# Performance work log

Hardware: AMD Instinct MI355X
Metric: run time of the kernel (lower is better)

The kernel has to match this reference:

```python
import jax, jax.numpy as jnp
import numpy as np

B, T, C, H, S = 8, 2048, 1024, 16, 64
EPS = 1e-5


def layernorm(x, g, b):
    m = jnp.mean(x, axis=-1, keepdims=True)
    v = jnp.mean((x - m) ** 2, axis=-1, keepdims=True)
    return (x - m) * jax.lax.rsqrt(v + EPS) * g + b


def wkv6(r, k, v, time_decay, u):
    # r,k,v: [B,T,H,S]; time_decay,u: [H,S]
    # kernel receives ew=-exp(w) and uses decay = exp(ew) = exp(-exp(w))
    d = jnp.exp(-jnp.exp(time_decay))  # [H,S], in (0,1)

    def step(state, rkv):
        r_t, k_t, v_t = rkv  # each [B,H,S]
        kv = k_t[..., :, None] * v_t[..., None, :]  # [B,H,S,S] outer product
        y = jnp.einsum('bhk,bhkv->bhv', r_t, state + u[None, :, :, None] * kv)
        state = state * d[None, :, :, None] + kv
        return state, y

    s0 = jnp.zeros((B, H, S, S), r.dtype)
    rkv_tm = (jnp.moveaxis(r, 1, 0), jnp.moveaxis(k, 1, 0), jnp.moveaxis(v, 1, 0))
    _, ys = jax.lax.scan(step, s0, rkv_tm)  # ys: [T,B,H,S]
    return jnp.moveaxis(ys, 0, 1).reshape(B, T, C)


def setup_inputs() -> dict:
    key = jax.random.key(0)
    ks = jax.random.split(key, 10)
    sc = C ** -0.5
    return {
        'x': jax.random.normal(ks[0], (B, T, C), jnp.float32),
        'time_decay': -5.0 + 0.5 * jax.random.normal(ks[1], (H, S), jnp.float32),
        'time_first': 0.1 * jax.random.normal(ks[2], (H, S), jnp.float32),
        'w_r': sc * jax.random.normal(ks[3], (C, C), jnp.float32),
        'w_k': sc * jax.random.normal(ks[4], (C, C), jnp.float32),
        'w_v': sc * jax.random.normal(ks[5], (C, C), jnp.float32),
        'w_o': sc * jax.random.normal(ks[6], (C, C), jnp.float32),
        'w_fk': sc * jax.random.normal(ks[7], (C, 4 * C), jnp.float32),
        'w_fv': (4 * C) ** -0.5 * jax.random.normal(ks[8], (4 * C, C), jnp.float32),
        'g1': jnp.ones((C,), jnp.float32),
        'b1': jnp.zeros((C,), jnp.float32),
        'g2': jnp.ones((C,), jnp.float32),
        'b2': jnp.zeros((C,), jnp.float32),
    }


def reference(x, time_decay, time_first, w_r, w_k, w_v, w_o, w_fk, w_fv, g1, b1, g2, b2):
    x_ln = layernorm(x, g1, b1)
    r = (x_ln @ w_r).reshape(B, T, H, S)
    k = (x_ln @ w_k).reshape(B, T, H, S)
    v = (x_ln @ w_v).reshape(B, T, H, S)
    wkv = wkv6(r, k, v, time_decay, time_first)  # [B,T,C]
    rwkv = jax.nn.sigmoid(r.reshape(B, T, C)) * wkv
    x = x + rwkv @ w_o
    x_ln2 = layernorm(x, g2, b2)
    ffn = (jax.nn.relu(x_ln2 @ w_fk) ** 2) @ w_fv
    return x + ffn
```

## Files before the change

kernel.cpp:

```cpp
#include <hip/hip_runtime.h>
#include <hip/hip_bf16.h>

#define B_ 8
#define T_ 2048
#define C_ 1024
#define H_ 16
#define S_ 64
#define BT_ (B_*T_)
#define FF_ (4*C_)
#define NC_ 32

typedef __attribute__((ext_vector_type(8))) short short8;
typedef __attribute__((ext_vector_type(4))) float f32x4;

union U8 { uint4 v; unsigned short s[8]; };

static __device__ __forceinline__ unsigned short f2bf(float f){
  unsigned u = __float_as_uint(f);
  unsigned r = (u + 0x7fffu + ((u >> 16) & 1u)) >> 16;
  return (unsigned short)r;
}
static __device__ __forceinline__ float bf2f(unsigned short u){
  return __uint_as_float(((unsigned)u) << 16);
}

static __device__ __forceinline__ void gll16(const unsigned short* g, unsigned short* l){
  __builtin_amdgcn_global_load_lds((const __attribute__((address_space(1))) void*)g,
                                   (__attribute__((address_space(3))) void*)l, 16, 0, 0);
}

__global__ __launch_bounds__(256) void ln_kernel(const float* __restrict__ x,
    const float* __restrict__ g, const float* __restrict__ b,
    unsigned short* __restrict__ out){
  int row = blockIdx.x;
  int tid = threadIdx.x;
  const float4* xr = reinterpret_cast<const float4*>(x + (size_t)row * C_);
  float4 v = xr[tid];
  float s = v.x + v.y + v.z + v.w;
  float q = v.x*v.x + v.y*v.y + v.z*v.z + v.w*v.w;
  int lane = tid & 63, w = tid >> 6;
  #pragma unroll
  for (int off = 32; off; off >>= 1){ s += __shfl_down(s, off); q += __shfl_down(q, off); }
  __shared__ float red[2][4];
  if (lane == 0){ red[0][w] = s; red[1][w] = q; }
  __syncthreads();
  s = red[0][0] + red[0][1] + red[0][2] + red[0][3];
  q = red[1][0] + red[1][1] + red[1][2] + red[1][3];
  float mean = s * (1.0f / C_);
  float var  = q * (1.0f / C_) - mean * mean;
  float inv = rsqrtf(var + 1e-5f);
  float4 gg = reinterpret_cast<const float4*>(g)[tid];
  float4 bb = reinterpret_cast<const float4*>(b)[tid];
  ushort4 o;
  o.x = f2bf((v.x - mean) * inv * gg.x + bb.x);
  o.y = f2bf((v.y - mean) * inv * gg.y + bb.y);
  o.z = f2bf((v.z - mean) * inv * gg.z + bb.z);
  o.w = f2bf((v.w - mean) * inv * gg.w + bb.w);
  reinterpret_cast<ushort4*>(out + (size_t)row * C_)[tid] = o;
}

__global__ __launch_bounds__(256) void wconv_kernel(const float* __restrict__ w,
    unsigned short* __restrict__ wt, int K, int N){
  __shared__ float tile[32][33];
  int bk = blockIdx.x * 32, bn = blockIdx.y * 32;
  int tx = threadIdx.x & 31, ty = threadIdx.x >> 5;
  #pragma unroll
  for (int i = 0; i < 4; i++)
    tile[ty + 8*i][tx] = w[(size_t)(bk + ty + 8*i) * N + bn + tx];
  __syncthreads();
  #pragma unroll
  for (int i = 0; i < 4; i++)
    wt[(size_t)(bn + ty + 8*i) * K + bk + tx] = f2bf(tile[tx][ty + 8*i]);
}

#define EPI_RKV3 1
#define EPI_WO   2
#define EPI_FK   3
#define EPI_FV   4

template<int EPI>
__global__ __launch_bounds__(512, 2) void gemm64_kernel(
    const unsigned short* __restrict__ A,
    const unsigned short* __restrict__ Bt,
    void* __restrict__ outp,
    const float* __restrict__ aux,
    int K, int nx){
  __shared__ unsigned short As[2][256][64];
  __shared__ unsigned short Bs[2][256][64];
  const int tid = threadIdx.x;

  int nwg = gridDim.x;
  int id  = blockIdx.x;
  id = (id & 7) * (nwg >> 3) + (id >> 3);
  int gsz = nx << 2;
  int g = id / gsz, rem = id % gsz;
  const int bm = ((g << 2) + (rem & 3)) * 256;
  const int bn = (rem >> 2) * 256;

  const int lane = tid & 63, wid = tid >> 6;
  const int wr = wid >> 2, wc = wid & 3;
  const int ml = lane & 15, hi = lane >> 4;

  const int srow  = lane >> 3;
  const int gslot = (lane & 7) ^ srow;

  auto stageA13 = [&](int bf, int kt){
    const size_t ko = (size_t)kt * 64 + gslot * 8;
    gll16(A + (size_t)(bm +  64 + wid*8 + srow) * K + ko, &As[bf][ 64 + wid*8][0]);
    gll16(A + (size_t)(bm + 192 + wid*8 + srow) * K + ko, &As[bf][192 + wid*8][0]);
  };
  auto stageA02 = [&](int bf, int kt){
    const size_t ko = (size_t)kt * 64 + gslot * 8;
    gll16(A + (size_t)(bm +       wid*8 + srow) * K + ko, &As[bf][      wid*8][0]);
    gll16(A + (size_t)(bm + 128 + wid*8 + srow) * K + ko, &As[bf][128 + wid*8][0]);
  };
  auto stageB4 = [&](int bf, int kt){
    const size_t ko = (size_t)kt * 64 + gslot * 8;
    #pragma unroll
    for (int s = 0; s < 4; s++)
      gll16(Bt + (size_t)(bn + s*64 + wid*8 + srow) * K + ko, &Bs[bf][s*64 + wid*8][0]);
  };

  auto lda = [&](int bf, int mf, int kk) -> short8 {
    return *(const short8*)&As[bf][wr*128 + mf*16 + ml][(((kk<<2)+hi) ^ (ml&7)) << 3];
  };
  auto ldb = [&](int bf, int nf, int kk) -> short8 {
    return *(const short8*)&Bs[bf][wc*64 + nf*16 + ml][(((kk<<2)+hi) ^ (ml&7)) << 3];
  };

  f32x4 acc[8][4];
  #pragma unroll
  for (int i = 0; i < 8; i++)
    #pragma unroll
    for (int j = 0; j < 4; j++)
      acc[i][j] = (f32x4){0.f, 0.f, 0.f, 0.f};

  const int NT = K >> 6;
  stageA02(0, 0); stageB4(0, 0);
  stageA13(0, 0);
  stageA02(1, 1); stageB4(1, 1);
  asm volatile("s_waitcnt vmcnt(8)" ::: "memory");
  __builtin_amdgcn_s_barrier();

  for (int kt = 0; kt < NT; ++kt){
    const int bf = kt & 1, nbf = bf ^ 1;
    const int k1 = (kt+1 < NT) ? kt+1 : kt;
    const int k2 = (kt+2 < NT) ? kt+2 : kt;
    short8 bfr[2][4];
    #pragma unroll
    for (int kk = 0; kk < 2; kk++)
      #pragma unroll
      for (int nf = 0; nf < 4; nf++)
        bfr[kk][nf] = ldb(bf, nf, kk);
    short8 af0[2][4];
    #pragma unroll
    for (int kk = 0; kk < 2; kk++)
      #pragma unroll
      for (int mf = 0; mf < 4; mf++)
        af0[kk][mf] = lda(bf, mf, kk);
    stageA13(nbf, k1);
    __builtin_amdgcn_s_setprio(1);
    #pragma unroll
    for (int mf = 0; mf < 4; mf++)
      #pragma unroll
      for (int kk = 0; kk < 2; kk++)
        #pragma unroll
        for (int nf = 0; nf < 4; nf++)
          acc[mf][nf] = __builtin_amdgcn_mfma_f32_16x16x32_bf16(af0[kk][mf], bfr[kk][nf], acc[mf][nf], 0, 0, 0);
    __builtin_amdgcn_s_setprio(0);
    asm volatile("s_waitcnt vmcnt(8) lgkmcnt(0)" ::: "memory");
    __builtin_amdgcn_s_barrier();
    short8 af1[2][4];
    #pragma unroll
    for (int kk = 0; kk < 2; kk++)
      #pragma unroll
      for (int mf = 0; mf < 4; mf++)
        af1[kk][mf] = lda(bf, 4+mf, kk);
    stageA02(bf, k2);
    stageB4(bf, k2);
    __builtin_amdgcn_s_setprio(1);
    #pragma unroll
    for (int mf = 0; mf < 4; mf++)
      #pragma unroll
      for (int kk = 0; kk < 2; kk++)
        #pragma unroll
        for (int nf = 0; nf < 4; nf++)
          acc[4+mf][nf] = __builtin_amdgcn_mfma_f32_16x16x32_bf16(af1[kk][mf], bfr[kk][nf], acc[4+mf][nf], 0, 0, 0);
    __builtin_amdgcn_s_setprio(0);
    asm volatile("s_waitcnt vmcnt(8) lgkmcnt(0)" ::: "memory");
    __builtin_amdgcn_s_barrier();
  }
  asm volatile("s_waitcnt vmcnt(0)" ::: "memory");

  const int rbase = bm + wr*128 + hi*4;
  const int cbase = bn + wc*64 + ml;
  #pragma unroll
  for (int mf = 0; mf < 8; mf++){
    #pragma unroll
    for (int nf = 0; nf < 4; nf++){
      #pragma unroll
      for (int r = 0; r < 4; r++){
        int m = rbase + mf*16 + r;
        int n = cbase + nf*16;
        float vv = acc[mf][nf][r];
        if (EPI == EPI_RKV3){
          unsigned short* o = (unsigned short*)outp;
          int b = m >> 11, t = m & (T_ - 1);
          int which = n >> 10, h = (n >> 6) & (H_ - 1), s = n & (S_ - 1);
          o[(size_t)which * BT_ * C_ + (((size_t)(b * H_ + h)) * T_ + t) * S_ + s] = f2bf(vv);
        } else if (EPI == EPI_WO){
          float* o = (float*)outp;
          o[(size_t)m * C_ + n] = aux[(size_t)m * C_ + n] + vv;
        } else if (EPI == EPI_FK){
          unsigned short* o = (unsigned short*)outp;
          float rl = vv > 0.f ? vv : 0.f;
          o[(size_t)m * FF_ + n] = f2bf(rl * rl);
        } else {
          float* o = (float*)outp;
          o[(size_t)m * C_ + n] += vv;
        }
      }
    }
  }
}


__global__ __launch_bounds__(256) void wkv_p1(
    const unsigned short* __restrict__ kT, const unsigned short* __restrict__ vT,
    const float* __restrict__ td, unsigned short* __restrict__ AS){
  const int bid = blockIdx.x;
  const int bh = bid >> 5, c = bid & (NC_ - 1);
  const int h = bh & (H_ - 1);
  const int tid = threadIdx.x, lane = tid & 63, w = tid >> 6;
  __shared__ unsigned short kh[64][72];
  __shared__ unsigned short vt[64][72];
  __shared__ float eps[64];
  if (tid < 64) eps[tid] = expf(td[h * S_ + tid]);
  __syncthreads();
  const int t = tid >> 2, q = (tid & 3) * 16;
  const size_t base = ((size_t)bh * T_ + c * 64 + t) * S_ + q;
  U8 k0, k1, v0, v1;
  k0.v = *(const uint4*)(kT + base);  k1.v = *(const uint4*)(kT + base + 8);
  v0.v = *(const uint4*)(vT + base);  v1.v = *(const uint4*)(vT + base + 8);
  const float mt = -(float)(63 - t);
  #pragma unroll
  for (int j = 0; j < 8; j++){
    int k = q + j;
    kh[k][t] = f2bf(bf2f(k0.s[j]) * expf(mt * eps[k]));
    vt[k][t] = v0.s[j];
  }
  #pragma unroll
  for (int j = 0; j < 8; j++){
    int k = q + 8 + j;
    kh[k][t] = f2bf(bf2f(k1.s[j]) * expf(mt * eps[k]));
    vt[k][t] = v1.s[j];
  }
  __syncthreads();
  const int ml = lane & 15, klo = (lane >> 4) * 8;
  f32x4 acc[4];
  #pragma unroll
  for (int nf = 0; nf < 4; nf++) acc[nf] = (f32x4){0.f,0.f,0.f,0.f};
  #pragma unroll
  for (int ks = 0; ks < 2; ks++){
    short8 af = *(const short8*)&vt[w*16 + ml][ks*32 + klo];
    #pragma unroll
    for (int nf = 0; nf < 4; nf++){
      short8 bfr = *(const short8*)&kh[nf*16 + ml][ks*32 + klo];
      acc[nf] = __builtin_amdgcn_mfma_f32_16x16x32_bf16(af, bfr, acc[nf], 0, 0, 0);
    }
  }
  unsigned short* dst = AS + ((size_t)bid * 64 + w*16 + (lane >> 4) * 4) * 64;
  #pragma unroll
  for (int nf = 0; nf < 4; nf++)
    #pragma unroll
    for (int r = 0; r < 4; r++)
      dst[(size_t)r * 64 + nf*16 + ml] = f2bf(acc[nf][r]);
}

__global__ __launch_bounds__(256) void wkv_p2(
    unsigned short* __restrict__ AS, const float* __restrict__ td){
  const int bh = blockIdx.x >> 2, vs = blockIdx.x & 3;
  const int h = bh & (H_ - 1);
  const int tid = threadIdx.x;
  const int vo = tid >> 4, k4 = (tid & 15) * 4;
  const int v = vs * 16 + vo;
  float dL[4], S[4];
  #pragma unroll
  for (int j = 0; j < 4; j++){
    dL[j] = expf(-64.f * expf(td[h * S_ + k4 + j]));
    S[j] = 0.f;
  }
  const size_t rb = ((size_t)bh * NC_ * 64 + v) * 64 + k4;
  for (int c = 0; c < NC_; c++){
    unsigned short* p = AS + rb + (size_t)c * 4096;
    ushort4 A = *(const ushort4*)p;
    ushort4 o;
    o.x = f2bf(S[0]); o.y = f2bf(S[1]); o.z = f2bf(S[2]); o.w = f2bf(S[3]);
    *(ushort4*)p = o;
    S[0] = fmaf(S[0], dL[0], bf2f(A.x)); S[1] = fmaf(S[1], dL[1], bf2f(A.y));
    S[2] = fmaf(S[2], dL[2], bf2f(A.z)); S[3] = fmaf(S[3], dL[3], bf2f(A.w));
  }
}

__global__ __launch_bounds__(256) void wkv_p3(
    const unsigned short* __restrict__ rT, const unsigned short* __restrict__ kT,
    const unsigned short* __restrict__ vT, const unsigned short* __restrict__ Sb,
    const float* __restrict__ td, const float* __restrict__ tf,
    unsigned short* __restrict__ rwkv){
  const int bid = blockIdx.x;
  const int bh = bid >> 5, c = bid & (NC_ - 1);
  const int b = bh >> 4, h = bh & (H_ - 1);
  const int tid = threadIdx.x, lane = tid & 63, w = tid >> 6;
  __shared__ unsigned short Rt[64][72];
  __shared__ unsigned short Kt[64][72];
  __shared__ unsigned short Vt[64][72];
  __shared__ unsigned short Sc[64][72];
  __shared__ float eps[64], us[64], diag[64];
  __shared__ float dred[64][4];

  if (tid < 64){ eps[tid] = expf(td[h * S_ + tid]); us[tid] = tf[h * S_ + tid]; }
  __syncthreads();

  const int t = tid >> 2, q = (tid & 3) * 16;
  const size_t base  = ((size_t)bh * T_ + c * 64 + t) * S_ + q;
  const size_t sbase = (((size_t)bh * NC_ + c) * 64 + t) * 64 + q;
  {
    U8 r0, r1, k0, k1, v0, v1, s0, s1, rt0, rt1, kt0, kt1;
    r0.v = *(const uint4*)(rT + base);  r1.v = *(const uint4*)(rT + base + 8);
    k0.v = *(const uint4*)(kT + base);  k1.v = *(const uint4*)(kT + base + 8);
    v0.v = *(const uint4*)(vT + base);  v1.v = *(const uint4*)(vT + base + 8);
    s0.v = *(const uint4*)(Sb + sbase); s1.v = *(const uint4*)(Sb + sbase + 8);
    float dpart = 0.f;
    const float ft = (float)t;
    #pragma unroll
    for (int j = 0; j < 8; j++){
      int k = q + j;
      float ep = eps[k];
      float rv = bf2f(r0.s[j]), kv = bf2f(k0.s[j]);
      rt0.s[j] = f2bf(rv * expf(-ft * ep));
      kt0.s[j] = f2bf(kv * expf((ft + 1.f) * ep));
      dpart = fmaf(rv * us[k], kv, dpart);
      Vt[k][t] = v0.s[j];
    }
    #pragma unroll
    for (int j = 0; j < 8; j++){
      int k = q + 8 + j;
      float ep = eps[k];
      float rv = bf2f(r1.s[j]), kv = bf2f(k1.s[j]);
      rt1.s[j] = f2bf(rv * expf(-ft * ep));
      kt1.s[j] = f2bf(kv * expf((ft + 1.f) * ep));
      dpart = fmaf(rv * us[k], kv, dpart);
      Vt[k][t] = v1.s[j];
    }
    *(uint4*)&Rt[t][q]     = rt0.v;  *(uint4*)&Rt[t][q + 8] = rt1.v;
    *(uint4*)&Kt[t][q]     = kt0.v;  *(uint4*)&Kt[t][q + 8] = kt1.v;
    *(uint4*)&Sc[t][q]     = s0.v;   *(uint4*)&Sc[t][q + 8] = s1.v;
    dred[t][tid & 3] = dpart;
  }
  __syncthreads();
  if (tid < 64) diag[tid] = dred[tid][0] + dred[tid][1] + dred[tid][2] + dred[tid][3];

  const int ml = lane & 15, klo = (lane >> 4) * 8;
  f32x4 acc1[4];
  #pragma unroll
  for (int nf = 0; nf < 4; nf++) acc1[nf] = (f32x4){0.f,0.f,0.f,0.f};
  #pragma unroll
  for (int ks = 0; ks < 2; ks++){
    short8 af = *(const short8*)&Rt[w*16 + ml][ks*32 + klo];
    #pragma unroll
    for (int nf = 0; nf < 4; nf++){
      short8 bfr = *(const short8*)&Kt[nf*16 + ml][ks*32 + klo];
      acc1[nf] = __builtin_amdgcn_mfma_f32_16x16x32_bf16(af, bfr, acc1[nf], 0, 0, 0);
    }
  }
  __syncthreads();

  #pragma unroll
  for (int nf = 0; nf < 4; nf++){
    #pragma unroll
    for (int r = 0; r < 4; r++){
      int tt = w*16 + (lane >> 4) * 4 + r;
      int ii = nf*16 + ml;
      float e = acc1[nf][r];
      float val = (ii < tt) ? e : (ii == tt ? diag[tt] : 0.f);
      Kt[tt][ii] = f2bf(val);
    }
  }
  __syncthreads();

  f32x4 acc2[4];
  #pragma unroll
  for (int nf = 0; nf < 4; nf++) acc2[nf] = (f32x4){0.f,0.f,0.f,0.f};
  #pragma unroll
  for (int ks = 0; ks < 2; ks++){
    short8 aA = *(const short8*)&Kt[w*16 + ml][ks*32 + klo];
    short8 aR = *(const short8*)&Rt[w*16 + ml][ks*32 + klo];
    #pragma unroll
    for (int nf = 0; nf < 4; nf++){
      short8 bV = *(const short8*)&Vt[nf*16 + ml][ks*32 + klo];
      acc2[nf] = __builtin_amdgcn_mfma_f32_16x16x32_bf16(aA, bV, acc2[nf], 0, 0, 0);
      short8 bS = *(const short8*)&Sc[nf*16 + ml][ks*32 + klo];
      acc2[nf] = __builtin_amdgcn_mfma_f32_16x16x32_bf16(aR, bS, acc2[nf], 0, 0, 0);
    }
  }

  const size_t rrow = ((size_t)bh * T_ + c * 64) * S_;
  #pragma unroll
  for (int nf = 0; nf < 4; nf++){
    #pragma unroll
    for (int r = 0; r < 4; r++){
      int tt = w*16 + (lane >> 4) * 4 + r;
      int vv = nf*16 + ml;
      float y = acc2[nf][r];
      float rv = bf2f(rT[rrow + (size_t)tt * S_ + vv]);
      float sig = 1.f / (1.f + expf(-rv));
      rwkv[((size_t)b * T_ + c * 64 + tt) * C_ + h * S_ + vv] = f2bf(sig * y);
    }
  }
}

extern "C" void kernel_launch(void* const* d_in, const int* in_sizes, int n_in,
                              void* d_out, int out_size, void* d_ws, size_t ws_size,
                              hipStream_t stream){
  const float* x    = (const float*)d_in[0];
  const float* td   = (const float*)d_in[1];
  const float* tf   = (const float*)d_in[2];
  const float* w_r  = (const float*)d_in[3];
  const float* w_k  = (const float*)d_in[4];
  const float* w_v  = (const float*)d_in[5];
  const float* w_o  = (const float*)d_in[6];
  const float* w_fk = (const float*)d_in[7];
  const float* w_fv = (const float*)d_in[8];
  const float* g1   = (const float*)d_in[9];
  const float* b1   = (const float*)d_in[10];
  const float* g2   = (const float*)d_in[11];
  const float* b2   = (const float*)d_in[12];
  float* out = (float*)d_out;

  char* ws = (char*)d_ws;
  size_t off = 0;
  auto alloc = [&](size_t bytes){ char* p = ws + off; off += (bytes + 255) & ~(size_t)255; return p; };
  unsigned short* wrT  = (unsigned short*)alloc((size_t)C_ * C_ * 2);
  unsigned short* wkT  = (unsigned short*)alloc((size_t)C_ * C_ * 2);
  unsigned short* wvT  = (unsigned short*)alloc((size_t)C_ * C_ * 2);
  unsigned short* woT  = (unsigned short*)alloc((size_t)C_ * C_ * 2);
  unsigned short* wfkT = (unsigned short*)alloc((size_t)C_ * FF_ * 2);
  unsigned short* wfvT = (unsigned short*)alloc((size_t)FF_ * C_ * 2);
  unsigned short* xln  = (unsigned short*)alloc((size_t)BT_ * C_ * 2);
  unsigned short* rT   = (unsigned short*)alloc((size_t)BT_ * C_ * 2);
  unsigned short* kT   = (unsigned short*)alloc((size_t)BT_ * C_ * 2);
  unsigned short* vT   = (unsigned short*)alloc((size_t)BT_ * C_ * 2);
  unsigned short* rwkv = (unsigned short*)alloc((size_t)BT_ * C_ * 2);
  unsigned short* hbuf = rT;
  unsigned short* AS   = xln;

  dim3 blk(256);
  dim3 blk5(512);

  wconv_kernel<<<dim3(C_/32,  C_/32),  blk, 0, stream>>>(w_r,  wrT,  C_,  C_);
  wconv_kernel<<<dim3(C_/32,  C_/32),  blk, 0, stream>>>(w_k,  wkT,  C_,  C_);
  wconv_kernel<<<dim3(C_/32,  C_/32),  blk, 0, stream>>>(w_v,  wvT,  C_,  C_);
  wconv_kernel<<<dim3(C_/32,  C_/32),  blk, 0, stream>>>(w_o,  woT,  C_,  C_);
  wconv_kernel<<<dim3(C_/32,  FF_/32), blk, 0, stream>>>(w_fk, wfkT, C_,  FF_);
  wconv_kernel<<<dim3(FF_/32, C_/32),  blk, 0, stream>>>(w_fv, wfvT, FF_, C_);

  ln_kernel<<<BT_, blk, 0, stream>>>(x, g1, b1, xln);

  gemm64_kernel<EPI_RKV3><<<dim3((3*C_/256)*(BT_/256)), blk5, 0, stream>>>(xln, wrT, rT, nullptr, C_, 3*C_/256);

  wkv_p1<<<B_*H_*NC_, blk, 0, stream>>>(kT, vT, td, AS);
  wkv_p2<<<B_*H_*4,   blk, 0, stream>>>(AS, td);
  wkv_p3<<<B_*H_*NC_, blk, 0, stream>>>(rT, kT, vT, AS, td, tf, rwkv);

  gemm64_kernel<EPI_WO><<<dim3((C_/256)*(BT_/256)), blk5, 0, stream>>>(rwkv, woT, out, x, C_, C_/256);

  ln_kernel<<<BT_, blk, 0, stream>>>(out, g2, b2, xln);

  gemm64_kernel<EPI_FK><<<dim3((FF_/256)*(BT_/256)), blk5, 0, stream>>>(xln, wfkT, hbuf, nullptr, C_, FF_/256);
  gemm64_kernel<EPI_FV><<<dim3((C_/256)*(BT_/256)), blk5, 0, stream>>>(hbuf, wfvT, out, nullptr, FF_, C_/256);
}
```

Baseline: 558.8 us.

## Switch GEMM to 32x32x16 MFMA tiles and batch weight conversions into one launch

```diff
diff --git a/kernel.cpp b/kernel.cpp
--- a/kernel.cpp
+++ b/kernel.cpp
@@ -12,6 +12,7 @@
 
 typedef __attribute__((ext_vector_type(8))) short short8;
 typedef __attribute__((ext_vector_type(4))) float f32x4;
+typedef __attribute__((ext_vector_type(16))) float f32x16;
 
 union U8 { uint4 v; unsigned short s[8]; };
 
@@ -59,10 +60,31 @@
   reinterpret_cast<ushort4*>(out + (size_t)row * C_)[tid] = o;
 }
 
-__global__ __launch_bounds__(256) void wconv_kernel(const float* __restrict__ w,
-    unsigned short* __restrict__ wt, int K, int N){
+__global__ __launch_bounds__(256) void wconv6_kernel(
+    const float* __restrict__ w0, const float* __restrict__ w1,
+    const float* __restrict__ w2, const float* __restrict__ w3,
+    const float* __restrict__ w4, const float* __restrict__ w5,
+    unsigned short* __restrict__ d0, unsigned short* __restrict__ d1,
+    unsigned short* __restrict__ d2, unsigned short* __restrict__ d3,
+    unsigned short* __restrict__ d4, unsigned short* __restrict__ d5){
   __shared__ float tile[32][33];
-  int bk = blockIdx.x * 32, bn = blockIdx.y * 32;
+  const int idx = blockIdx.x;
+  const float* w; unsigned short* wt; int K, N, bk, bn;
+  if (idx < 4096){
+    int which = idx >> 10, i = idx & 1023;
+    w  = which==0 ? w0 : which==1 ? w1 : which==2 ? w2 : w3;
+    wt = which==0 ? d0 : which==1 ? d1 : which==2 ? d2 : d3;
+    K = 1024; N = 1024;
+    bk = (i & 31) * 32; bn = (i >> 5) * 32;
+  } else if (idx < 8192){
+    int i = idx - 4096;
+    w = w4; wt = d4; K = 1024; N = 4096;
+    bk = (i & 31) * 32; bn = (i >> 5) * 32;
+  } else {
+    int i = idx - 8192;
+    w = w5; wt = d5; K = 4096; N = 1024;
+    bk = (i & 127) * 32; bn = (i >> 7) * 32;
+  }
   int tx = threadIdx.x & 31, ty = threadIdx.x >> 5;
   #pragma unroll
   for (int i = 0; i < 4; i++)
@@ -99,7 +121,7 @@
 
   const int lane = tid & 63, wid = tid >> 6;
   const int wr = wid >> 2, wc = wid & 3;
-  const int ml = lane & 15, hi = lane >> 4;
+  const int l31 = lane & 31, khalf = lane >> 5;
 
   const int srow  = lane >> 3;
   const int gslot = (lane & 7) ^ srow;
@@ -122,18 +144,20 @@
   };
 
   auto lda = [&](int bf, int mf, int kk) -> short8 {
-    return *(const short8*)&As[bf][wr*128 + mf*16 + ml][(((kk<<2)+hi) ^ (ml&7)) << 3];
+    return *(const short8*)&As[bf][wr*128 + mf*32 + l31][(((kk<<1)+khalf) ^ (l31&7)) << 3];
   };
   auto ldb = [&](int bf, int nf, int kk) -> short8 {
-    return *(const short8*)&Bs[bf][wc*64 + nf*16 + ml][(((kk<<2)+hi) ^ (ml&7)) << 3];
+    return *(const short8*)&Bs[bf][wc*64 + nf*32 + l31][(((kk<<1)+khalf) ^ (l31&7)) << 3];
   };
 
-  f32x4 acc[8][4];
-  #pragma unroll
-  for (int i = 0; i < 8; i++)
-    #pragma unroll
-    for (int j = 0; j < 4; j++)
-      acc[i][j] = (f32x4){0.f, 0.f, 0.f, 0.f};
+  f32x16 acc[4][2];
+  #pragma unroll
+  for (int i = 0; i < 4; i++)
+    #pragma unroll
+    for (int j = 0; j < 2; j++)
+      #pragma unroll
+      for (int e = 0; e < 16; e++)
+        acc[i][j][e] = 0.f;
 
   const int NT = K >> 6;
   stageA02(0, 0); stageB4(0, 0);
@@ -146,63 +170,62 @@
     const int bf = kt & 1, nbf = bf ^ 1;
     const int k1 = (kt+1 < NT) ? kt+1 : kt;
     const int k2 = (kt+2 < NT) ? kt+2 : kt;
-    short8 bfr[2][4];
-    #pragma unroll
-    for (int kk = 0; kk < 2; kk++)
-      #pragma unroll
-      for (int nf = 0; nf < 4; nf++)
+    short8 bfr[4][2];
+    #pragma unroll
+    for (int kk = 0; kk < 4; kk++)
+      #pragma unroll
+      for (int nf = 0; nf < 2; nf++)
         bfr[kk][nf] = ldb(bf, nf, kk);
-    short8 af0[2][4];
-    #pragma unroll
-    for (int kk = 0; kk < 2; kk++)
-      #pragma unroll
-      for (int mf = 0; mf < 4; mf++)
+    short8 af0[4][2];
+    #pragma unroll
+    for (int kk = 0; kk < 4; kk++)
+      #pragma unroll
+      for (int mf = 0; mf < 2; mf++)
         af0[kk][mf] = lda(bf, mf, kk);
     stageA13(nbf, k1);
     __builtin_amdgcn_s_setprio(1);
     #pragma unroll
-    for (int mf = 0; mf < 4; mf++)
-      #pragma unroll
-      for (int kk = 0; kk < 2; kk++)
+    for (int mf = 0; mf < 2; mf++)
+      #pragma unroll
+      for (int kk = 0; kk < 4; kk++)
         #pragma unroll
-        for (int nf = 0; nf < 4; nf++)
-          acc[mf][nf] = __builtin_amdgcn_mfma_f32_16x16x32_bf16(af0[kk][mf], bfr[kk][nf], acc[mf][nf], 0, 0, 0);
+        for (int nf = 0; nf < 2; nf++)
+          acc[mf][nf] = __builtin_amdgcn_mfma_f32_32x32x16_bf16(af0[kk][mf], bfr[kk][nf], acc[mf][nf], 0, 0, 0);
     __builtin_amdgcn_s_setprio(0);
     asm volatile("s_waitcnt vmcnt(8) lgkmcnt(0)" ::: "memory");
     __builtin_amdgcn_s_barrier();
-    short8 af1[2][4];
-    #pragma unroll
-    for (int kk = 0; kk < 2; kk++)
-      #pragma unroll
-      for (int mf = 0; mf < 4; mf++)
-        af1[kk][mf] = lda(bf, 4+mf, kk);
+    short8 af1[4][2];
+    #pragma unroll
+    for (int kk = 0; kk < 4; kk++)
+      #pragma unroll
+      for (int mf = 0; mf < 2; mf++)
+        af1[kk][mf] = lda(bf, 2+mf, kk);
     stageA02(bf, k2);
     stageB4(bf, k2);
     __builtin_amdgcn_s_setprio(1);
     #pragma unroll
-    for (int mf = 0; mf < 4; mf++)
-      #pragma unroll
-      for (int kk = 0; kk < 2; kk++)
+    for (int mf = 0; mf < 2; mf++)
+      #pragma unroll
+      for (int kk = 0; kk < 4; kk++)
         #pragma unroll
-        for (int nf = 0; nf < 4; nf++)
-          acc[4+mf][nf] = __builtin_amdgcn_mfma_f32_16x16x32_bf16(af1[kk][mf], bfr[kk][nf], acc[4+mf][nf], 0, 0, 0);
+        for (int nf = 0; nf < 2; nf++)
+          acc[2+mf][nf] = __builtin_amdgcn_mfma_f32_32x32x16_bf16(af1[kk][mf], bfr[kk][nf], acc[2+mf][nf], 0, 0, 0);
     __builtin_amdgcn_s_setprio(0);
     asm volatile("s_waitcnt vmcnt(8) lgkmcnt(0)" ::: "memory");
     __builtin_amdgcn_s_barrier();
   }
   asm volatile("s_waitcnt vmcnt(0)" ::: "memory");
 
-  const int rbase = bm + wr*128 + hi*4;
-  const int cbase = bn + wc*64 + ml;
-  #pragma unroll
-  for (int mf = 0; mf < 8; mf++){
-    #pragma unroll
-    for (int nf = 0; nf < 4; nf++){
-      #pragma unroll
-      for (int r = 0; r < 4; r++){
-        int m = rbase + mf*16 + r;
-        int n = cbase + nf*16;
-        float vv = acc[mf][nf][r];
+  const int rquad = khalf * 4;
+  #pragma unroll
+  for (int mf = 0; mf < 4; mf++){
+    #pragma unroll
+    for (int nf = 0; nf < 2; nf++){
+      #pragma unroll
+      for (int reg = 0; reg < 16; reg++){
+        int m = bm + wr*128 + mf*32 + (reg & 3) + 8*(reg >> 2) + rquad;
+        int n = bn + wc*64 + nf*32 + l31;
+        float vv = acc[mf][nf][reg];
         if (EPI == EPI_RKV3){
           unsigned short* o = (unsigned short*)outp;
           int b = m >> 11, t = m & (T_ - 1);
@@ -457,12 +480,8 @@
   dim3 blk(256);
   dim3 blk5(512);
 
-  wconv_kernel<<<dim3(C_/32,  C_/32),  blk, 0, stream>>>(w_r,  wrT,  C_,  C_);
-  wconv_kernel<<<dim3(C_/32,  C_/32),  blk, 0, stream>>>(w_k,  wkT,  C_,  C_);
-  wconv_kernel<<<dim3(C_/32,  C_/32),  blk, 0, stream>>>(w_v,  wvT,  C_,  C_);
-  wconv_kernel<<<dim3(C_/32,  C_/32),  blk, 0, stream>>>(w_o,  woT,  C_,  C_);
-  wconv_kernel<<<dim3(C_/32,  FF_/32), blk, 0, stream>>>(w_fk, wfkT, C_,  FF_);
-  wconv_kernel<<<dim3(FF_/32, C_/32),  blk, 0, stream>>>(w_fv, wfvT, FF_, C_);
+  wconv6_kernel<<<dim3(12288), blk, 0, stream>>>(w_r, w_k, w_v, w_o, w_fk, w_fv,
+                                                 wrT, wkT, wvT, woT, wfkT, wfvT);
 
   ln_kernel<<<BT_, blk, 0, stream>>>(x, g1, b1, xln);
 
```

Result: slower. 584.9 us (+4.7%).
